# Kernel tuning notes

Hardware: AMD Instinct MI355X
Metric: run time of the kernel (lower is better)

Reference implementation:

```python
import jax, jax.numpy as jnp
import numpy as np

EPS = 1e-6

def _rms_norm(x, w):
    # torch: x / (||x||_2 * n^{-1/2} + eps) * w
    rms = jnp.linalg.norm(x, axis=-1, keepdims=True) * (x.shape[-1] ** -0.5)
    return x / (rms + EPS) * w

def _rope_cos_sin(seq_len, head_dim):
    half = head_dim // 2
    freq = 1.0 / (10000.0 ** (jnp.arange(half, dtype=jnp.float32) / half))
    t = jnp.arange(seq_len, dtype=jnp.float32)
    freqs = t[:, None] * freq[None, :]            # [s, half]
    freqs = jnp.concatenate([freqs, freqs], -1)   # [s, d_head]
    cos = jnp.cos(freqs)[None, :, None, :]        # [1, s, 1, d_head]
    sin = jnp.sin(freqs)[None, :, None, :]
    return cos, sin

def _rotate_half(x):
    h = x.shape[-1] // 2
    return jnp.concatenate([-x[..., h:], x[..., :h]], -1)

def setup_inputs() -> dict:
    key = jax.random.key(0)
    ks = jax.random.split(key, 8)
    B, S, D, H, F = 2, 2048, 2048, 16, 128
    return {
        'query_input': jax.random.normal(ks[0], (B, S, D), jnp.float32),
        'key_input':   jax.random.normal(ks[1], (B, S, D), jnp.float32),
        'value_input': jax.random.normal(ks[2], (B, S, D), jnp.float32),
        'W_Q': jax.random.normal(ks[3], (H, D, F), jnp.float32) * (D ** -0.5),
        'W_K': jax.random.normal(ks[4], (H, D, F), jnp.float32) * (D ** -0.5),
        'W_V': jax.random.normal(ks[5], (H, D, F), jnp.float32) * (D ** -0.5),
        'W_O': jax.random.normal(ks[6], (H, F, D), jnp.float32) * (F ** -0.5),
        'b_Q': jnp.zeros((H, F), jnp.float32),
        'b_K': jnp.zeros((H, F), jnp.float32),
        'b_V': jnp.zeros((H, F), jnp.float32),
        'b_O': jnp.zeros((D,), jnp.float32),
        'q_norm_w': jnp.ones((F,), jnp.float32),
        'k_norm_w': jnp.ones((F,), jnp.float32),
    }

def reference(query_input, key_input, value_input, W_Q, W_K, W_V, W_O,
              b_Q, b_K, b_V, b_O, q_norm_w, k_norm_w):
    head_dim = W_Q.shape[-1]
    q = jnp.einsum('bpd,hdf->bphf', query_input, W_Q) + b_Q[None, None]
    k = jnp.einsum('bpd,hdf->bphf', key_input,   W_K) + b_K[None, None]
    v = jnp.einsum('bpd,hdf->bphf', value_input, W_V) + b_V[None, None]
    q = _rms_norm(q, q_norm_w)
    k = _rms_norm(k, k_norm_w)
    cos, sin = _rope_cos_sin(q.shape[1], head_dim)
    q = q * cos + _rotate_half(q) * sin
    k = k * cos + _rotate_half(k) * sin
    scores = jnp.einsum('bphf,bqhf->bhpq', q, k) / (head_dim ** 0.5)
    pattern = jax.nn.softmax(scores, axis=-1)
    attn = jnp.einsum('bhpq,bqhf->bphf', pattern, v)
    return jnp.einsum('bphf,hfm->bpm', attn, W_O) + b_O
```

## Files before the change

### kernel.cpp

```cpp
#include <hip/hip_runtime.h>
#include <stdint.h>

typedef unsigned short u16;
typedef __attribute__((ext_vector_type(8))) short  s8b;
typedef __attribute__((ext_vector_type(4))) float  f32x4;

#define S_LEN   2048
#define NHEAD   16
#define HD      128
#define DM      2048
#define NB      2
#define NPLANE  (NB*NHEAD)
#define ROWS    (NB*S_LEN)
#define PLANE_ELEMS (S_LEN*HD)
#define ATT_SCALE 0.08838834764831845f
#define LOG2E     1.4426950408889634f

__device__ __forceinline__ float bf2f(u16 u){
  union { unsigned u; float f; } x; x.u = ((unsigned)u) << 16; return x.f;
}
__device__ __forceinline__ u16 f2bf(float f){
  union { float f; unsigned u; } x; x.f = f;
  unsigned r = x.u + 0x7FFFu + ((x.u >> 16) & 1u);
  return (u16)(r >> 16);
}
__device__ __forceinline__ unsigned cvtpk(float lo, float hi){
  unsigned r;
  asm("v_cvt_pk_bf16_f32 %0, %1, %2" : "=v"(r) : "v"(lo), "v"(hi));
  return r;
}

typedef const __attribute__((address_space(1))) unsigned int* gas1;
typedef __attribute__((address_space(3))) unsigned int* las3;
__device__ __forceinline__ void gload16(const void* g, void* l){
  __builtin_amdgcn_global_load_lds((gas1)g, (las3)l, 16, 0, 0);
}

__device__ __forceinline__ f32x4 mfma16(s8b a, s8b b, f32x4 c){
  return __builtin_amdgcn_mfma_f32_16x16x32_bf16(a, b, c, 0, 0, 0);
}

__global__ __launch_bounds__(256) void cvt4x3(const float4* __restrict__ a,
                                              const float4* __restrict__ b,
                                              const float4* __restrict__ c,
                                              uint2* __restrict__ oa,
                                              uint2* __restrict__ ob,
                                              uint2* __restrict__ oc, int n4){
  int i = blockIdx.x*256 + threadIdx.x;
  if (i >= n4) return;
  const float4* src = (blockIdx.y == 0) ? a : (blockIdx.y == 1) ? b : c;
  uint2*       dst  = (blockIdx.y == 0) ? oa : (blockIdx.y == 1) ? ob : oc;
  float4 v = src[i];
  uint2 o;
  o.x = (unsigned)f2bf(v.x) | ((unsigned)f2bf(v.y) << 16);
  o.y = (unsigned)f2bf(v.z) | ((unsigned)f2bf(v.w) << 16);
  dst[i] = o;
}

__global__ __launch_bounds__(256) void transpose_all(const float* __restrict__ WQ,
                                                     const float* __restrict__ WK,
                                                     const float* __restrict__ WV,
                                                     const float* __restrict__ WO,
                                                     u16* __restrict__ WqT,
                                                     u16* __restrict__ WkT,
                                                     u16* __restrict__ WvT,
                                                     u16* __restrict__ WoT){
  __shared__ float tile[32][33];
  int u = blockIdx.x;
  int mat = u >> 12, rem = u & 4095;
  const float* in; u16* out; int R, C, outStride, z, r0, c0;
  if (mat == 0){
    in = WO; out = WoT; R = 2048; C = 2048; outStride = 2048; z = 0;
    r0 = (rem & 63)*32; c0 = (rem >> 6)*32;
  } else {
    in  = (mat == 1) ? WQ  : (mat == 2) ? WK  : WV;
    out = (mat == 1) ? WqT : (mat == 2) ? WkT : WvT;
    R = 2048; C = 128; outStride = 2048;
    z  = rem >> 8;
    r0 = (rem & 63)*32; c0 = ((rem >> 6) & 3)*32;
  }
  const float* inz = in + (size_t)z * R * C;
  u16* outz = out + (size_t)z * C * outStride;
  int tx = threadIdx.x & 31, ty = threadIdx.x >> 5;
  #pragma unroll
  for (int i=0;i<4;i++)
    tile[ty*4+i][tx] = inz[(size_t)(r0+ty*4+i)*C + c0 + tx];
  __syncthreads();
  #pragma unroll
  for (int i=0;i<4;i++)
    outz[(size_t)(c0+ty*4+i)*outStride + r0 + tx] = f2bf(tile[tx][ty*4+i]);
}

__global__ __launch_bounds__(256) void rope_tab(float* __restrict__ ctab,
                                                float* __restrict__ stab){
  int i = blockIdx.x*256 + threadIdx.x;
  int p = i >> 6, j = i & 63;
  float freq = exp2f(-(float)j * (13.287712379549449f/64.0f));
  float a = (float)p * freq;
  ctab[i] = cosf(a);
  stab[i] = sinf(a);
}

__device__ __forceinline__ void gemm_core(u16* lds,
                                          const u16* __restrict__ A,
                                          const u16* __restrict__ BT,
                                          const float* __restrict__ bias,
                                          void* __restrict__ out, int mode){
  const int K = 2048;
  const int NT = 32;
  const int t = threadIdx.x, w = t >> 6, l = t & 63;
  const int lr = l & 15, lg = l >> 4;
  const int wr = w >> 1, wc = w & 1;
  int bid = blockIdx.x;
  int swz = (bid & 7)*32 + (bid >> 3);
  const int M0 = (swz >> 4) * 256, N0 = (swz & 15) * 128;

  f32x4 acc[4][4];
  #pragma unroll
  for (int i=0;i<4;i++)
    #pragma unroll
    for (int j=0;j<4;j++) acc[i][j] = f32x4{0.f,0.f,0.f,0.f};

  auto stageH = [&](int ttu, int h){
    int slot = (2*ttu + h) % 6;
    int tt   = ttu & 31;
    char* base = (char*)&lds[slot*12288];
    #pragma unroll
    for (int j=0;j<2;j++){
      int d = w*2048 + j*1024 + l*16;
      int row = d >> 7;
      int koff = ((l&7)*16) ^ ((row&7)<<4);
      gload16((const char*)A + ((size_t)(M0 + h*128 + row)*K + tt*64)*2 + koff,
              base + w*2048 + j*1024);
    }
    {
      int d = w*1024 + l*16;
      int row = d >> 7;
      int koff = ((l&7)*16) ^ ((row&7)<<4);
      gload16((const char*)BT + ((size_t)(N0 + h*64 + row)*K + tt*64)*2 + koff,
              base + 16384 + w*1024);
    }
  };

  stageH(0,0); stageH(0,1); stageH(1,0); stageH(1,1);

  for (int kt=0; kt<NT; kt++){
    const char* Ab = (const char*)&lds[((2*kt + (wr>>1)) % 6)*12288];
    const char* Bb = (const char*)&lds[((2*kt + wc) % 6)*12288] + 16384;

    stageH(kt+2, 0);
    asm volatile("s_waitcnt vmcnt(9)" ::: "memory");
    __builtin_amdgcn_s_barrier();
    __builtin_amdgcn_sched_barrier(0);

    s8b af[4][2];
    #pragma unroll
    for (int mi=0;mi<4;mi++)
      #pragma unroll
      for (int kc=0;kc<2;kc++){
        int rA = (wr&1)*64 + mi*16 + lr;
        af[mi][kc] = *(const s8b*)(Ab + rA*128 + ((kc*64 + lg*16) ^ ((rA&7)<<4)));
      }
    {
      s8b bf[2][2];
      #pragma unroll
      for (int nj=0;nj<2;nj++){
        int rB = nj*16 + lr;
        bf[nj][0] = *(const s8b*)(Bb + rB*128 + ((0*64 + lg*16) ^ ((rB&7)<<4)));
        bf[nj][1] = *(const s8b*)(Bb + rB*128 + ((1*64 + lg*16) ^ ((rB&7)<<4)));
      }
      __builtin_amdgcn_s_setprio(1);
      #pragma unroll
      for (int mi=0;mi<4;mi++)
        #pragma unroll
        for (int nj=0;nj<2;nj++){
          acc[mi][nj] = mfma16(af[mi][0], bf[nj][0], acc[mi][nj]);
          acc[mi][nj] = mfma16(af[mi][1], bf[nj][1], acc[mi][nj]);
        }
      __builtin_amdgcn_s_setprio(0);
    }
    stageH(kt+2, 1);
    {
      s8b bf[2][2];
      #pragma unroll
      for (int nj=0;nj<2;nj++){
        int rB = (nj+2)*16 + lr;
        bf[nj][0] = *(const s8b*)(Bb + rB*128 + ((0*64 + lg*16) ^ ((rB&7)<<4)));
        bf[nj][1] = *(const s8b*)(Bb + rB*128 + ((1*64 + lg*16) ^ ((rB&7)<<4)));
      }
      __builtin_amdgcn_s_setprio(1);
      #pragma unroll
      for (int mi=0;mi<4;mi++)
        #pragma unroll
        for (int nj=0;nj<2;nj++){
          acc[mi][nj+2] = mfma16(af[mi][0], bf[nj][0], acc[mi][nj+2]);
          acc[mi][nj+2] = mfma16(af[mi][1], bf[nj][1], acc[mi][nj+2]);
        }
      __builtin_amdgcn_s_setprio(0);
    }
    __builtin_amdgcn_sched_barrier(0);
    __builtin_amdgcn_s_barrier();
    __builtin_amdgcn_sched_barrier(0);
  }
  asm volatile("s_waitcnt vmcnt(0)" ::: "memory");

  #pragma unroll
  for (int mi=0;mi<4;mi++){
    int growb = M0 + wr*64 + mi*16 + lg*4;
    #pragma unroll
    for (int nj=0;nj<4;nj++){
      int gcol = N0 + wc*64 + nj*16 + lr;
      float bv = bias[gcol];
      #pragma unroll
      for (int r=0;r<4;r++){
        int grow = growb + r;
        float v = acc[mi][nj][r] + bv;
        if (mode == 2){
          ((float*)out)[(size_t)grow*2048 + gcol] = v;
        } else {
          int b = grow >> 11, p = grow & 2047;
          int h = gcol >> 7,  f = gcol & 127;
          if (mode == 0){
            ((u16*)out)[(((size_t)(b*NHEAD+h))*S_LEN + p)*HD + f] = f2bf(v);
          } else {
            size_t base = ((size_t)(b*NHEAD+h)*PLANE_ELEMS)*2 + (size_t)(p>>6)*16384;
            int p6 = p & 63;
            int q_ = ((p6&12)<<1) | (p6&3) | ((p6&16)>>2);
            int kvp = (p6 & 32) | q_;
            int kc = kvp >> 5, lgv = (kvp >> 3) & 3, jv = kvp & 7;
            int off = (kc*8 + (f>>4))*1024 + (lgv*16 + (f&15))*16 + jv*2;
            *(u16*)((char*)out + base + off) = f2bf(v);
          }
        }
      }
    }
  }
}

__global__ __launch_bounds__(512) void gemm_qkv(const u16* __restrict__ Aq,
                                                const u16* __restrict__ Ak,
                                                const u16* __restrict__ Av,
                                                const u16* __restrict__ Bq,
                                                const u16* __restrict__ Bk,
                                                const u16* __restrict__ Bv,
                                                const float* __restrict__ bq,
                                                const float* __restrict__ bk,
                                                const float* __restrict__ bv,
                                                void* __restrict__ oq,
                                                void* __restrict__ ok,
                                                void* __restrict__ ov){
  __shared__ u16 lds[6*12288];
  int y = blockIdx.y;
  const u16* A  = (y==0) ? Aq : (y==1) ? Ak : Av;
  const u16* BT = (y==0) ? Bq : (y==1) ? Bk : Bv;
  const float* bias = (y==0) ? bq : (y==1) ? bk : bv;
  void* out = (y==0) ? oq : (y==1) ? ok : ov;
  int mode = (y==2) ? 1 : 0;
  gemm_core(lds, A, BT, bias, out, mode);
}

__global__ __launch_bounds__(512) void gemm_bt(const u16* __restrict__ A,
                                               const u16* __restrict__ BT,
                                               const float* __restrict__ bias,
                                               void* __restrict__ out, int mode){
  __shared__ u16 lds[6*12288];
  gemm_core(lds, A, BT, bias, out, mode);
}

__global__ __launch_bounds__(256) void norm_rope2(const u16* __restrict__ qin,
                                                  u16* __restrict__ qout,
                                                  const float* __restrict__ qwv,
                                                  const u16* __restrict__ kin,
                                                  u16* __restrict__ kout,
                                                  const float* __restrict__ kwv,
                                                  const float* __restrict__ ctab,
                                                  const float* __restrict__ stab,
                                                  float qscale){
  int t = threadIdx.x, w = t>>6, l = t&63;
  int isK = blockIdx.y;
  const u16* in  = isK ? kin  : qin;
  u16*       outp= isK ? kout : qout;
  const float* nw= isK ? kwv  : qwv;
  float oscale   = isK ? 1.0f : qscale;
  size_t R = (size_t)blockIdx.x*4 + w;
  int p = (int)(R & (S_LEN-1));
  size_t base = R * HD;
  float x0 = bf2f(in[base + l]);
  float x1 = bf2f(in[base + 64 + l]);
  float ss = x0*x0 + x1*x1;
  #pragma unroll
  for (int m=1;m<64;m<<=1) ss += __shfl_xor(ss, m);
  float rms = sqrtf(ss * (1.0f/128.0f));
  float sc = oscale / (rms + 1e-6f);
  float xn0 = x0 * sc * nw[l];
  float xn1 = x1 * sc * nw[64+l];
  float c = ctab[(size_t)p*64 + l], s = stab[(size_t)p*64 + l];
  float o0 = xn0*c - xn1*s;
  float o1 = xn1*c + xn0*s;
  if (!isK){
    outp[base + l]      = f2bf(o0);
    outp[base + 64 + l] = f2bf(o1);
  } else {
    size_t plane = R >> 11;
    int kv = p & 63;
    size_t tb = (plane*(size_t)PLANE_ELEMS + (size_t)(p>>6)*8192) * 2;
    int b0 = (kv*256 + l*2)        ^ ((kv&7)<<4);
    int b1 = (kv*256 + (64+l)*2)   ^ ((kv&7)<<4);
    *(u16*)((char*)outp + tb + b0) = f2bf(o0);
    *(u16*)((char*)outp + tb + b1) = f2bf(o1);
  }
}

__global__ __launch_bounds__(256,2) void attn_fwd(const u16* __restrict__ qn,
                                                  const u16* __restrict__ kn,
                                                  const u16* __restrict__ vt,
                                                  u16* __restrict__ attn_out){
  __shared__ u16 Klds[2][8192];
  int t = threadIdx.x, w = t>>6, l = t&63;
  int lr = l&15, lg = l>>4;

  int bid = blockIdx.x;
  int xcd = bid & 7, j = bid >> 3;
  int plane = xcd*4 + (j >> 4);
  int qb = j & 15;
  int q0 = qb*128 + w*32;

  const s8b ones = { (short)0x3F80, (short)0x3F80, (short)0x3F80, (short)0x3F80,
                     (short)0x3F80, (short)0x3F80, (short)0x3F80, (short)0x3F80 };

  s8b qf[2][4];
  #pragma unroll
  for (int qi=0; qi<2; qi++)
    #pragma unroll
    for (int fc=0; fc<4; fc++)
      qf[qi][fc] = *(const s8b*)(qn + ((size_t)plane*S_LEN + q0 + qi*16 + lr)*HD + fc*32 + lg*8);

  f32x4 lacc[2];
  lacc[0] = f32x4{0.f,0.f,0.f,0.f};
  lacc[1] = f32x4{0.f,0.f,0.f,0.f};
  f32x4 oacc[2][8];
  #pragma unroll
  for (int qi=0;qi<2;qi++)
    #pragma unroll
    for (int i=0;i<8;i++) oacc[qi][i] = f32x4{0.f,0.f,0.f,0.f};

  const u16* kbase = kn + (size_t)plane*PLANE_ELEMS;
  const char* vbase = (const char*)vt + (size_t)plane*PLANE_ELEMS*2;

  auto stage = [&](int buf, int kt){
    #pragma unroll
    for (int i=0;i<4;i++)
      gload16(kbase + (size_t)kt*8192 + w*2048 + i*512 + l*8, &Klds[buf][w*2048 + i*512]);
  };

  stage(0, 0);
  int cur = 0;
  for (int kt=0; kt<32; kt++){
    __syncthreads();
    if (kt+1 < 32) stage(cur^1, kt+1);

    const char* vb = vbase + (size_t)kt*16384;
    s8b vf0[8];
    #pragma unroll
    for (int fc2=0; fc2<8; fc2++)
      vf0[fc2] = *(const s8b*)(vb + fc2*1024 + l*16);

    f32x4 sacc[4][2];
    #pragma unroll
    for (int c=0;c<4;c++){
      sacc[c][0] = f32x4{0.f,0.f,0.f,0.f};
      sacc[c][1] = f32x4{0.f,0.f,0.f,0.f};
    }
    __builtin_amdgcn_s_setprio(1);
    #pragma unroll
    for (int c=0;c<4;c++){
      int kv = c*16 + lr;
      #pragma unroll
      for (int fc=0; fc<4; fc++){
        int byte = (kv*256 + (fc*32 + lg*8)*2) ^ ((kv&7)<<4);
        s8b kf = *(const s8b*)((const char*)&Klds[cur][0] + byte);
        sacc[c][0] = mfma16(kf, qf[0][fc], sacc[c][0]);
        sacc[c][1] = mfma16(kf, qf[1][fc], sacc[c][1]);
      }
    }
    __builtin_amdgcn_s_setprio(0);

    s8b vf1[8];
    #pragma unroll
    for (int fc2=0; fc2<8; fc2++)
      vf1[fc2] = *(const s8b*)(vb + (8+fc2)*1024 + l*16);

    float pv[2][4][4];
    #pragma unroll
    for (int qi=0;qi<2;qi++)
      #pragma unroll
      for (int c=0;c<4;c++){
        pv[qi][c][0] = exp2f(sacc[c][qi][0]);
        pv[qi][c][1] = exp2f(sacc[c][qi][1]);
        pv[qi][c][2] = exp2f(sacc[c][qi][2]);
        pv[qi][c][3] = exp2f(sacc[c][qi][3]);
      }

    s8b pa[2][2];
    #pragma unroll
    for (int qi=0;qi<2;qi++)
      #pragma unroll
      for (int kc=0;kc<2;kc++){
        union { s8b v; unsigned u[4]; } pu;
        pu.u[0] = cvtpk(pv[qi][2*kc][0],   pv[qi][2*kc][1]);
        pu.u[1] = cvtpk(pv[qi][2*kc][2],   pv[qi][2*kc][3]);
        pu.u[2] = cvtpk(pv[qi][2*kc+1][0], pv[qi][2*kc+1][1]);
        pu.u[3] = cvtpk(pv[qi][2*kc+1][2], pv[qi][2*kc+1][3]);
        pa[qi][kc] = pu.v;
      }

    __builtin_amdgcn_s_setprio(1);
    lacc[0] = mfma16(pa[0][0], ones, lacc[0]);
    lacc[1] = mfma16(pa[1][0], ones, lacc[1]);
    #pragma unroll
    for (int fc2=0; fc2<8; fc2++){
      oacc[0][fc2] = mfma16(pa[0][0], vf0[fc2], oacc[0][fc2]);
      oacc[1][fc2] = mfma16(pa[1][0], vf0[fc2], oacc[1][fc2]);
    }
    lacc[0] = mfma16(pa[0][1], ones, lacc[0]);
    lacc[1] = mfma16(pa[1][1], ones, lacc[1]);
    #pragma unroll
    for (int fc2=0; fc2<8; fc2++){
      oacc[0][fc2] = mfma16(pa[0][1], vf1[fc2], oacc[0][fc2]);
      oacc[1][fc2] = mfma16(pa[1][1], vf1[fc2], oacc[1][fc2]);
    }
    __builtin_amdgcn_s_setprio(0);
    cur ^= 1;
  }

  int b = plane >> 4, h = plane & 15;
  #pragma unroll
  for (int qi=0;qi<2;qi++){
    float inv[4];
    #pragma unroll
    for (int r=0;r<4;r++) inv[r] = 1.0f / lacc[qi][r];
    #pragma unroll
    for (int fc2=0; fc2<8; fc2++){
      int f = fc2*16 + lr;
      #pragma unroll
      for (int r=0;r<4;r++){
        int row = q0 + qi*16 + lg*4 + r;
        float o = oacc[qi][fc2][r] * inv[r];
        attn_out[(((size_t)b*S_LEN + row)*NHEAD + h)*HD + f] = f2bf(o);
      }
    }
  }
}

extern "C" void kernel_launch(void* const* d_in, const int* in_sizes, int n_in,
                              void* d_out, int out_size, void* d_ws, size_t ws_size,
                              hipStream_t stream){
  const float* xq = (const float*)d_in[0];
  const float* xk = (const float*)d_in[1];
  const float* xv = (const float*)d_in[2];
  const float* WQ = (const float*)d_in[3];
  const float* WK = (const float*)d_in[4];
  const float* WV = (const float*)d_in[5];
  const float* WO = (const float*)d_in[6];
  const float* bQ = (const float*)d_in[7];
  const float* bK = (const float*)d_in[8];
  const float* bV = (const float*)d_in[9];
  const float* bO = (const float*)d_in[10];
  const float* qw = (const float*)d_in[11];
  const float* kw = (const float*)d_in[12];

  char* ws = (char*)d_ws;
  size_t off = 0;
  auto alloc = [&](size_t bytes)->void*{
    void* p = ws + off; off += (bytes + 255) & ~(size_t)255; return p;
  };
  const size_t ACT = (size_t)ROWS*DM*2;
  const size_t WMT = (size_t)DM*DM*2;
  u16* xqb  = (u16*)alloc(ACT);
  u16* xkb  = (u16*)alloc(ACT);
  u16* xvb  = (u16*)alloc(ACT);
  u16* WqT  = (u16*)alloc(WMT);
  u16* WkT  = (u16*)alloc(WMT);
  u16* WvT  = (u16*)alloc(WMT);
  u16* WoT  = (u16*)alloc(WMT);
  u16* qraw = (u16*)alloc(ACT);
  u16* kraw = (u16*)alloc(ACT);
  u16* knT  = (u16*)alloc(ACT);
  u16* vtS  = (u16*)alloc(ACT);
  u16* attn = (u16*)alloc(ACT);
  float* ctab = (float*)alloc((size_t)S_LEN*64*4);
  float* stab = (float*)alloc((size_t)S_LEN*64*4);
  if (off > ws_size) return;

  const int n4 = ROWS*DM/4;
  cvt4x3<<<dim3(n4/256, 3), dim3(256), 0, stream>>>((const float4*)xq, (const float4*)xk,
                                                    (const float4*)xv, (uint2*)xqb,
                                                    (uint2*)xkb, (uint2*)xvb, n4);
  rope_tab<<<dim3(S_LEN*64/256), dim3(256), 0, stream>>>(ctab, stab);
  transpose_all<<<dim3(4*4096), dim3(256), 0, stream>>>(WQ, WK, WV, WO, WqT, WkT, WvT, WoT);

  gemm_qkv<<<dim3(256,3), dim3(512), 0, stream>>>(xqb, xkb, xvb, WqT, WkT, WvT,
                                                  bQ, bK, bV, qraw, kraw, vtS);

  norm_rope2<<<dim3(NPLANE*S_LEN/4, 2), dim3(256), 0, stream>>>(qraw, qraw, qw,
                                                                kraw, knT, kw,
                                                                ctab, stab, ATT_SCALE*LOG2E);

  attn_fwd<<<dim3(512), dim3(256), 0, stream>>>(qraw, knT, vtS, attn);

  gemm_bt<<<dim3(256), dim3(512), 0, stream>>>(attn, WoT, bO, d_out, 2);
}
```

Measured before the change: 322.7 us.

## Fuse RMSNorm and RoPE into the Q/K projection GEMM epilogue

Removes the separate norm_rope2 kernel and performs bias add, per-head RMS norm, scaling and rotary embedding directly in the QKV GEMM epilogue. Each 128-wide N tile is exactly one head, so row sums of squares are reduced via shuffles and LDS across the two column warps. The normalized tile is staged in LDS so each lane can fetch its rotate-half partner. This drops a bf16 round-trip of Q and K through global memory plus a kernel launch, but adds barriers and LDS traffic to the GEMM tail.

```diff
diff --git a/kernel.cpp b/kernel.cpp
--- a/kernel.cpp
+++ b/kernel.cpp
@@ -105,7 +105,10 @@
                                           const u16* __restrict__ A,
                                           const u16* __restrict__ BT,
                                           const float* __restrict__ bias,
-                                          void* __restrict__ out, int mode){
+                                          void* __restrict__ out, int mode,
+                                          const float* __restrict__ nw,
+                                          const float* __restrict__ ctab,
+                                          const float* __restrict__ stab){
   const int K = 2048;
   const int NT = 32;
   const int t = threadIdx.x, w = t >> 6, l = t & 63;
@@ -204,6 +207,82 @@
   }
   asm volatile("s_waitcnt vmcnt(0)" ::: "memory");
 
+  if (mode == 0 || mode == 3){
+    __builtin_amdgcn_s_barrier();
+    float* xn_lds = (float*)lds;
+    float* rs_lds = (float*)((char*)lds + 133120);
+    const int h = N0 >> 7;
+    float nwv[4];
+    #pragma unroll
+    for (int nj=0;nj<4;nj++) nwv[nj] = nw[wc*64 + nj*16 + lr];
+    #pragma unroll
+    for (int nj=0;nj<4;nj++){
+      float bv = bias[N0 + wc*64 + nj*16 + lr];
+      #pragma unroll
+      for (int mi=0;mi<4;mi++)
+        #pragma unroll
+        for (int r=0;r<4;r++) acc[mi][nj][r] += bv;
+    }
+    #pragma unroll
+    for (int mi=0;mi<4;mi++)
+      #pragma unroll
+      for (int r=0;r<4;r++){
+        float s = acc[mi][0][r]*acc[mi][0][r] + acc[mi][1][r]*acc[mi][1][r]
+                + acc[mi][2][r]*acc[mi][2][r] + acc[mi][3][r]*acc[mi][3][r];
+        s += __shfl_xor(s,1); s += __shfl_xor(s,2);
+        s += __shfl_xor(s,4); s += __shfl_xor(s,8);
+        int row = wr*64 + mi*16 + lg*4 + r;
+        rs_lds[row*2 + wc] = s;
+      }
+    __builtin_amdgcn_s_barrier();
+    const float oscale = (mode==0) ? (ATT_SCALE*LOG2E) : 1.0f;
+    float scx[4][4];
+    #pragma unroll
+    for (int mi=0;mi<4;mi++)
+      #pragma unroll
+      for (int r=0;r<4;r++){
+        int row = wr*64 + mi*16 + lg*4 + r;
+        float ss = rs_lds[row*2] + rs_lds[row*2+1];
+        scx[mi][r] = oscale / (sqrtf(ss * (1.0f/128.0f)) + 1e-6f);
+      }
+    #pragma unroll
+    for (int mi=0;mi<4;mi++)
+      #pragma unroll
+      for (int nj=0;nj<4;nj++)
+        #pragma unroll
+        for (int r=0;r<4;r++){
+          int row = wr*64 + mi*16 + lg*4 + r;
+          int col = wc*64 + nj*16 + lr;
+          xn_lds[row*130 + col] = acc[mi][nj][r] * scx[mi][r] * nwv[nj];
+        }
+    __builtin_amdgcn_s_barrier();
+    #pragma unroll
+    for (int mi=0;mi<4;mi++)
+      #pragma unroll
+      for (int nj=0;nj<4;nj++)
+        #pragma unroll
+        for (int r=0;r<4;r++){
+          int row = wr*64 + mi*16 + lg*4 + r;
+          int col = wc*64 + nj*16 + lr;
+          int grow = M0 + row;
+          int b = grow >> 11, p = grow & 2047;
+          float xo = xn_lds[row*130 + col];
+          float xp = xn_lds[row*130 + (col^64)];
+          float cz = ctab[p*64 + (col&63)], sz = stab[p*64 + (col&63)];
+          float o = wc ? (xo*cz + xp*sz) : (xo*cz - xp*sz);
+          if (mode == 0){
+            ((u16*)out)[(((size_t)(b*NHEAD+h))*S_LEN + p)*HD + col] = f2bf(o);
+          } else {
+            size_t plane = (size_t)(b*NHEAD+h);
+            int kv = p & 63;
+            size_t tb = (plane*(size_t)PLANE_ELEMS + (size_t)(p>>6)*8192) * 2;
+            int byt = (kv*256 + col*2) ^ ((kv&7)<<4);
+            *(u16*)((char*)out + tb + byt) = f2bf(o);
+          }
+        }
+    return;
+  }
+
   #pragma unroll
   for (int mi=0;mi<4;mi++){
     int growb = M0 + wr*64 + mi*16 + lg*4;
@@ -220,17 +299,13 @@
         } else {
           int b = grow >> 11, p = grow & 2047;
           int h = gcol >> 7,  f = gcol & 127;
-          if (mode == 0){
-            ((u16*)out)[(((size_t)(b*NHEAD+h))*S_LEN + p)*HD + f] = f2bf(v);
-          } else {
-            size_t base = ((size_t)(b*NHEAD+h)*PLANE_ELEMS)*2 + (size_t)(p>>6)*16384;
-            int p6 = p & 63;
-            int q_ = ((p6&12)<<1) | (p6&3) | ((p6&16)>>2);
-            int kvp = (p6 & 32) | q_;
-            int kc = kvp >> 5, lgv = (kvp >> 3) & 3, jv = kvp & 7;
-            int off = (kc*8 + (f>>4))*1024 + (lgv*16 + (f&15))*16 + jv*2;
-            *(u16*)((char*)out + base + off) = f2bf(v);
-          }
+          size_t base = ((size_t)(b*NHEAD+h)*PLANE_ELEMS)*2 + (size_t)(p>>6)*16384;
+          int p6 = p & 63;
+          int q_ = ((p6&12)<<1) | (p6&3) | ((p6&16)>>2);
+          int kvp = (p6 & 32) | q_;
+          int kc = kvp >> 5, lgv = (kvp >> 3) & 3, jv = kvp & 7;
+          int off = (kc*8 + (f>>4))*1024 + (lgv*16 + (f&15))*16 + jv*2;
+          *(u16*)((char*)out + base + off) = f2bf(v);
         }
       }
     }
@@ -248,15 +323,20 @@
                                                 const float* __restrict__ bv,
                                                 void* __restrict__ oq,
                                                 void* __restrict__ ok,
-                                                void* __restrict__ ov){
+                                                void* __restrict__ ov,
+                                                const float* __restrict__ qw,
+                                                const float* __restrict__ kw,
+                                                const float* __restrict__ ctab,
+                                                const float* __restrict__ stab){
   __shared__ u16 lds[6*12288];
   int y = blockIdx.y;
   const u16* A  = (y==0) ? Aq : (y==1) ? Ak : Av;
   const u16* BT = (y==0) ? Bq : (y==1) ? Bk : Bv;
   const float* bias = (y==0) ? bq : (y==1) ? bk : bv;
   void* out = (y==0) ? oq : (y==1) ? ok : ov;
-  int mode = (y==2) ? 1 : 0;
-  gemm_core(lds, A, BT, bias, out, mode);
+  int mode = (y==0) ? 0 : (y==1) ? 3 : 1;
+  const float* nw = (y==1) ? kw : qw;
+  gemm_core(lds, A, BT, bias, out, mode, nw, ctab, stab);
 }
 
 __global__ __launch_bounds__(512) void gemm_bt(const u16* __restrict__ A,
@@ -264,51 +344,7 @@
                                                const float* __restrict__ bias,
                                                void* __restrict__ out, int mode){
   __shared__ u16 lds[6*12288];
-  gemm_core(lds, A, BT, bias, out, mode);
-}
-
-__global__ __launch_bounds__(256) void norm_rope2(const u16* __restrict__ qin,
-                                                  u16* __restrict__ qout,
-                                                  const float* __restrict__ qwv,
-                                                  const u16* __restrict__ kin,
-                                                  u16* __restrict__ kout,
-                                                  const float* __restrict__ kwv,
-                                                  const float* __restrict__ ctab,
-                                                  const float* __restrict__ stab,
-                                                  float qscale){
-  int t = threadIdx.x, w = t>>6, l = t&63;
-  int isK = blockIdx.y;
-  const u16* in  = isK ? kin  : qin;
-  u16*       outp= isK ? kout : qout;
-  const float* nw= isK ? kwv  : qwv;
-  float oscale   = isK ? 1.0f : qscale;
-  size_t R = (size_t)blockIdx.x*4 + w;
-  int p = (int)(R & (S_LEN-1));
-  size_t base = R * HD;
-  float x0 = bf2f(in[base + l]);
-  float x1 = bf2f(in[base + 64 + l]);
-  float ss = x0*x0 + x1*x1;
-  #pragma unroll
-  for (int m=1;m<64;m<<=1) ss += __shfl_xor(ss, m);
-  float rms = sqrtf(ss * (1.0f/128.0f));
-  float sc = oscale / (rms + 1e-6f);
-  float xn0 = x0 * sc * nw[l];
-  float xn1 = x1 * sc * nw[64+l];
-  float c = ctab[(size_t)p*64 + l], s = stab[(size_t)p*64 + l];
-  float o0 = xn0*c - xn1*s;
-  float o1 = xn1*c + xn0*s;
-  if (!isK){
-    outp[base + l]      = f2bf(o0);
-    outp[base + 64 + l] = f2bf(o1);
-  } else {
-    size_t plane = R >> 11;
-    int kv = p & 63;
-    size_t tb = (plane*(size_t)PLANE_ELEMS + (size_t)(p>>6)*8192) * 2;
-    int b0 = (kv*256 + l*2)        ^ ((kv&7)<<4);
-    int b1 = (kv*256 + (64+l)*2)   ^ ((kv&7)<<4);
-    *(u16*)((char*)outp + tb + b0) = f2bf(o0);
-    *(u16*)((char*)outp + tb + b1) = f2bf(o1);
-  }
+  gemm_core(lds, A, BT, bias, out, mode, nullptr, nullptr, nullptr);
 }
 
 __global__ __launch_bounds__(256,2) void attn_fwd(const u16* __restrict__ qn,
@@ -484,7 +520,6 @@
   u16* WvT  = (u16*)alloc(WMT);
   u16* WoT  = (u16*)alloc(WMT);
   u16* qraw = (u16*)alloc(ACT);
-  u16* kraw = (u16*)alloc(ACT);
   u16* knT  = (u16*)alloc(ACT);
   u16* vtS  = (u16*)alloc(ACT);
   u16* attn = (u16*)alloc(ACT);
@@ -500,11 +535,8 @@
   transpose_all<<<dim3(4*4096), dim3(256), 0, stream>>>(WQ, WK, WV, WO, WqT, WkT, WvT, WoT);
 
   gemm_qkv<<<dim3(256,3), dim3(512), 0, stream>>>(xqb, xkb, xvb, WqT, WkT, WvT,
-                                                  bQ, bK, bV, qraw, kraw, vtS);
-
-  norm_rope2<<<dim3(NPLANE*S_LEN/4, 2), dim3(256), 0, stream>>>(qraw, qraw, qw,
-                                                                kraw, knT, kw,
-                                                                ctab, stab, ATT_SCALE*LOG2E);
+                                                  bQ, bK, bV, qraw, knT, vtS,
+                                                  qw, kw, ctab, stab);
 
   attn_fwd<<<dim3(512), dim3(256), 0, stream>>>(qraw, knT, vtS, attn);
 
```

After: 323.7 us. About the same (+0.3%).
